# Kernel tuning notes

Hardware: AMD Instinct MI355X
Metric: run time of the kernel (lower is better)

The kernel has to match this reference:

```python
import jax, jax.numpy as jnp
import numpy as np

HID = 1024
HEADS = 16
HEAD_DIM = HID // HEADS
FF = 4096
CAP = 0.125
AUXW = 0.01
ROPE_THETA = 10000.0


def setup_inputs() -> dict:
    key = jax.random.key(0)
    ks = jax.random.split(key, 12)
    B, T, D = 4, 4096, HID
    s = 0.02  # weight init scale
    return {
        "hidden_states": jax.random.normal(ks[0], (B, T, D), jnp.float32),
        "w_router": jax.random.normal(ks[1], (D, 1), jnp.float32) * s,
        "wq": jax.random.normal(ks[2], (D, D), jnp.float32) * s,
        "wk": jax.random.normal(ks[3], (D, D), jnp.float32) * s,
        "wv": jax.random.normal(ks[4], (D, D), jnp.float32) * s,
        "wo": jax.random.normal(ks[5], (D, D), jnp.float32) * s,
        "ln1_w": jnp.ones((D,), jnp.float32),
        "ln2_w": jnp.ones((D,), jnp.float32),
        "w_gate": jax.random.normal(ks[6], (D, FF), jnp.float32) * s,
        "w_up": jax.random.normal(ks[7], (D, FF), jnp.float32) * s,
        "w_down": jax.random.normal(ks[8], (FF, D), jnp.float32) * s,
    }


def _rmsnorm(x, w, eps=1e-6):
    var = jnp.mean(jnp.square(x), axis=-1, keepdims=True)
    return x * jax.lax.rsqrt(var + eps) * w


def _rope(x, pos):
    # x: [B,S,H,Dh], pos: [B,S] float positions (original token indices)
    Dh = x.shape[-1]
    inv_freq = 1.0 / (ROPE_THETA ** (jnp.arange(0, Dh, 2, dtype=jnp.float32) / Dh))
    ang = pos[..., None] * inv_freq            # [B,S,Dh/2]
    cos = jnp.cos(ang)[:, :, None, :]
    sin = jnp.sin(ang)[:, :, None, :]
    x1, x2 = x[..., : Dh // 2], x[..., Dh // 2:]
    return jnp.concatenate([x1 * cos - x2 * sin, x2 * cos + x1 * sin], axis=-1)


def reference(hidden_states, w_router, wq, wk, wv, wo, ln1_w, ln2_w, w_gate, w_up, w_down):
    B, T, D = hidden_states.shape
    kk = max(1, int(T * CAP))  # tokens selected per row (static)

    # ---- router ----
    logits = (hidden_states @ w_router)[..., 0]          # [B,T]
    _, topi = jax.lax.top_k(logits, kk)                  # [B,kk]
    bidx = jnp.arange(B)[:, None]
    # aux loss: BCE-with-logits vs binary top-k targets, mean over all B*T
    targets = jnp.zeros_like(logits).at[bidx, topi].set(1.0)
    aux_loss = jnp.mean(
        jnp.maximum(logits, 0.0) - logits * targets + jnp.log1p(jnp.exp(-jnp.abs(logits)))
    ) * AUXW

    # ---- select tokens (sorted by position to preserve causality) ----
    idx = jnp.sort(topi, axis=-1)                        # [B,kk]
    x_sel = hidden_states[bidx, idx]                     # [B,kk,D]
    gates = jax.nn.sigmoid(logits[bidx, idx])[..., None] # [B,kk,1]
    pos = idx.astype(jnp.float32)

    # ---- decoder block on selected tokens ----
    h = _rmsnorm(x_sel, ln1_w)
    q = (h @ wq).reshape(B, kk, HEADS, HEAD_DIM)
    k = (h @ wk).reshape(B, kk, HEADS, HEAD_DIM)
    v = (h @ wv).reshape(B, kk, HEADS, HEAD_DIM)
    q = _rope(q, pos)
    k = _rope(k, pos)
    scores = jnp.einsum("bqhd,bkhd->bhqk", q, k) / np.sqrt(HEAD_DIM)
    causal = jnp.tril(jnp.ones((kk, kk), dtype=bool))
    scores = jnp.where(causal, scores, jnp.finfo(scores.dtype).min)
    attn = jax.nn.softmax(scores, axis=-1)
    o = jnp.einsum("bhqk,bkhd->bqhd", attn, v).reshape(B, kk, D) @ wo
    x1 = x_sel + o
    h2 = _rmsnorm(x1, ln2_w)
    mlp = (jax.nn.silu(h2 @ w_gate) * (h2 @ w_up)) @ w_down
    block_out = x1 + mlp

    # ---- soft-gated scatter back ----
    new_sel = x_sel + gates * (block_out - x_sel)
    new_states = hidden_states.at[bidx, idx].set(new_sel)
    return new_states, aux_loss
```

## Files before the change

kernel.cpp:

```cpp
#include <hip/hip_runtime.h>
#include <math.h>

#define NB 4
#define NT 4096
#define ND 1024
#define NH 16
#define NDH 64
#define NFF 4096
#define NKK 512
#define NTOK (NB*NKK)
#define OUT_MAIN ((size_t)NB*NT*ND)

typedef unsigned short u16;
typedef __bf16 bf16x8 __attribute__((ext_vector_type(8)));
typedef short  s16x8  __attribute__((ext_vector_type(8)));
typedef unsigned short u16x4 __attribute__((ext_vector_type(4)));
typedef float  f32x4  __attribute__((ext_vector_type(4)));

__device__ inline u16 f2b(float f) {
    unsigned u = __builtin_bit_cast(unsigned, f);
    unsigned r = u + 0x7FFFu + ((u >> 16) & 1u);
    return (u16)(r >> 16);
}
__device__ inline float b2f(u16 v) {
    unsigned u = ((unsigned)v) << 16;
    return __builtin_bit_cast(float, u);
}

__global__ __launch_bounds__(256)
void router_kernel(const float* __restrict__ hs, const float* __restrict__ wr,
                   float* __restrict__ logits, float* __restrict__ partials)
{
    int wave = threadIdx.x >> 6, lane = threadIdx.x & 63;
    int row = blockIdx.x * 4 + wave;
    const float4* x4 = (const float4*)(hs + (size_t)row * ND);
    const float4* w4 = (const float4*)wr;
    float acc = 0.f;
#pragma unroll
    for (int i = 0; i < 4; ++i) {
        float4 a = x4[lane + i * 64];
        float4 b = w4[lane + i * 64];
        acc += a.x * b.x + a.y * b.y + a.z * b.z + a.w * b.w;
    }
    for (int off = 32; off; off >>= 1) acc += __shfl_down(acc, off);
    __shared__ float sp4[4];
    if (lane == 0) {
        logits[row] = acc;
        sp4[wave] = fmaxf(acc, 0.f) + log1pf(expf(-fabsf(acc)));
    }
    __syncthreads();
    if (threadIdx.x == 0)
        partials[blockIdx.x] = sp4[0] + sp4[1] + sp4[2] + sp4[3];
}

__global__ __launch_bounds__(1024)
void topk_kernel(const float* __restrict__ logits, int* __restrict__ idxv,
                 float* __restrict__ gates, float* __restrict__ S2)
{
    __shared__ unsigned key[NT];
    __shared__ unsigned hist[256];
    __shared__ unsigned wsum[16];
    __shared__ float red[16];
    __shared__ unsigned sh_pref, sh_r;
    int b = blockIdx.x, tid = threadIdx.x;
    int lane = tid & 63, wv = tid >> 6;
    const float* lg = logits + (size_t)b * NT;
    for (int i = tid; i < NT; i += 1024) {
        unsigned u = __float_as_uint(lg[i]);
        u ^= (u >> 31) ? 0xFFFFFFFFu : 0x80000000u;
        key[i] = u;
    }
    if (tid == 0) { sh_pref = 0u; sh_r = NKK; }
    if (tid < 256) hist[tid] = 0u;
    __syncthreads();
    unsigned prefmask = 0u;
#pragma unroll
    for (int pass = 0; pass < 4; ++pass) {
        int shift = 24 - 8 * pass;
        unsigned pm = prefmask, pref = sh_pref;
        for (int i = tid; i < NT; i += 1024) {
            unsigned kk = key[i];
            if ((kk & pm) == pref) atomicAdd(&hist[(kk >> shift) & 255u], 1u);
        }
        __syncthreads();
        if (tid == 0) {
            unsigned r = sh_r, cum = 0;
            for (int bin = 255; bin >= 0; --bin) {
                unsigned c = hist[bin];
                if (cum + c >= r) {
                    sh_pref = pref | ((unsigned)bin << shift);
                    sh_r = r - cum;
                    break;
                }
                cum += c;
            }
        }
        __syncthreads();
        if (tid < 256) hist[tid] = 0u;
        prefmask |= (255u << shift);
        __syncthreads();
    }
    unsigned kstar = sh_pref;
    unsigned r2 = sh_r;
    int base = tid * 4;
    unsigned g_loc[4], t_loc[4];
    unsigned tsum = 0;
#pragma unroll
    for (int j = 0; j < 4; ++j) {
        unsigned kk = key[base + j];
        g_loc[j] = (kk > kstar) ? 1u : 0u;
        t_loc[j] = (kk == kstar) ? 1u : 0u;
        tsum += t_loc[j];
    }
    unsigned x = tsum;
#pragma unroll
    for (int off = 1; off < 64; off <<= 1) {
        unsigned v = __shfl_up(x, off);
        if (lane >= off) x += v;
    }
    if (lane == 63) wsum[wv] = x;
    __syncthreads();
    if (tid == 0) {
        unsigned run = 0;
        for (int i = 0; i < 16; ++i) { unsigned t = wsum[i]; wsum[i] = run; run += t; }
    }
    __syncthreads();
    unsigned tie_run = wsum[wv] + x - tsum;
    unsigned s_loc[4], ssum = 0;
#pragma unroll
    for (int j = 0; j < 4; ++j) {
        unsigned sel = g_loc[j] | (t_loc[j] & ((tie_run < r2) ? 1u : 0u));
        tie_run += t_loc[j];
        s_loc[j] = sel;
        ssum += sel;
    }
    __syncthreads();
    unsigned y = ssum;
#pragma unroll
    for (int off = 1; off < 64; off <<= 1) {
        unsigned v = __shfl_up(y, off);
        if (lane >= off) y += v;
    }
    if (lane == 63) wsum[wv] = y;
    __syncthreads();
    if (tid == 0) {
        unsigned run = 0;
        for (int i = 0; i < 16; ++i) { unsigned t = wsum[i]; wsum[i] = run; run += t; }
    }
    __syncthreads();
    unsigned pos = wsum[wv] + y - ssum;
    float lsum = 0.f;
#pragma unroll
    for (int j = 0; j < 4; ++j) {
        if (s_loc[j]) {
            int gi = base + j;
            float l = lg[gi];
            idxv[b * NKK + pos] = gi;
            gates[b * NKK + pos] = 1.f / (1.f + expf(-l));
            lsum += l;
            ++pos;
        }
    }
    for (int off = 32; off; off >>= 1) lsum += __shfl_down(lsum, off);
    if (lane == 0) red[wv] = lsum;
    __syncthreads();
    if (tid == 0) {
        float t = 0.f;
        for (int i = 0; i < 16; ++i) t += red[i];
        atomicAdd(S2, t);
    }
}

__global__ __launch_bounds__(1024)
void aux_kernel(const float* __restrict__ partials, const float* __restrict__ S2,
                float* __restrict__ outp)
{
    int tid = threadIdx.x, lane = tid & 63, wv = tid >> 6;
    float s = 0.f;
    for (int i = tid; i < 4096; i += 1024) s += partials[i];
    for (int off = 32; off; off >>= 1) s += __shfl_down(s, off);
    __shared__ float red[16];
    if (lane == 0) red[wv] = s;
    __syncthreads();
    if (tid == 0) {
        float t = 0.f;
        for (int i = 0; i < 16; ++i) t += red[i];
        outp[0] = (t - S2[0]) * (0.01f / (float)(NB * NT));
    }
}

__global__ __launch_bounds__(256)
void transpose_conv(const float* __restrict__ src, u16* __restrict__ dst,
                    int K, int N)
{
    __shared__ u16 T[64][68];
    int n0 = blockIdx.x * 64, k0 = blockIdx.y * 64;
    int tid = threadIdx.x;
#pragma unroll
    for (int it = 0; it < 4; ++it) {
        int slot = it * 256 + tid;
        int k = slot >> 4, n4 = (slot & 15) * 4;
        float4 v = *(const float4*)&src[(size_t)(k0 + k) * N + n0 + n4];
        u16x4 o = { f2b(v.x), f2b(v.y), f2b(v.z), f2b(v.w) };
        *(u16x4*)&T[k][n4] = o;
    }
    __syncthreads();
#pragma unroll
    for (int it = 0; it < 2; ++it) {
        int slot = it * 256 + tid;
        int n = slot >> 3, k8 = (slot & 7) * 8;
        s16x8 o;
#pragma unroll
        for (int i = 0; i < 8; ++i) o[i] = (short)T[k8 + i][n];
        *(s16x8*)&dst[(size_t)(n0 + n) * K + k0 + k8] = o;
    }
}

template<int GATHER>
__global__ __launch_bounds__(256)
void rms_kernel(const float* __restrict__ src, const int* __restrict__ idxv,
                const float* __restrict__ w, float* __restrict__ xsel,
                u16* __restrict__ outp)
{
    int blk = blockIdx.x, tid = threadIdx.x;
    const float* x;
    if (GATHER) {
        int b = blk >> 9;
        x = src + ((size_t)b * NT + idxv[blk]) * ND;
    } else {
        x = src + (size_t)blk * ND;
    }
    float4 v = *(const float4*)&x[tid * 4];
    float ss = v.x * v.x + v.y * v.y + v.z * v.z + v.w * v.w;
    for (int off = 32; off; off >>= 1) ss += __shfl_down(ss, off);
    __shared__ float wred[4];
    if ((tid & 63) == 0) wred[tid >> 6] = ss;
    __syncthreads();
    float tot = wred[0] + wred[1] + wred[2] + wred[3];
    float scale = rsqrtf(tot * (1.f / (float)ND) + 1e-6f);
    float4 wv = *(const float4*)&w[tid * 4];
    u16x4 o = { f2b(v.x * scale * wv.x), f2b(v.y * scale * wv.y),
                f2b(v.z * scale * wv.z), f2b(v.w * scale * wv.w) };
    *(u16x4*)&outp[(size_t)blk * ND + tid * 4] = o;
    if (GATHER) *(float4*)&xsel[(size_t)blk * ND + tid * 4] = v;
}

#define LPAD 40
template<int EPI>
__global__ __launch_bounds__(256)
void gemm_bt(const u16* __restrict__ A, const u16* __restrict__ B,
             void* __restrict__ Cv, int K, int lda, int ldb, int ldc,
             const float* __restrict__ P1, const float* __restrict__ P2,
             const float* __restrict__ gates, const int* __restrict__ idxv,
             float* __restrict__ outp)
{
    __shared__ u16 As[128 * LPAD];
    __shared__ u16 Bs[128 * LPAD];
    int tid = threadIdx.x, lane = tid & 63, w = tid >> 6;
    int wr = w >> 1, wc = w & 1;
    int bm = blockIdx.y * 128, bn = blockIdx.x * 128;
    int arow = tid >> 2, acol = (tid & 3) * 8;
    const u16* Ap = A + (size_t)(bm + arow) * lda + acol;
    const u16* Ap2 = Ap + (size_t)64 * lda;
    const u16* Bp = B + (size_t)(bn + arow) * ldb + acol;
    const u16* Bp2 = Bp + (size_t)64 * ldb;
    int c15 = lane & 15, ks8 = (lane >> 4) * 8;
    int aoff[4], boff[4];
#pragma unroll
    for (int m2 = 0; m2 < 4; ++m2) aoff[m2] = (wr * 64 + m2 * 16 + c15) * LPAD + ks8;
#pragma unroll
    for (int n2 = 0; n2 < 4; ++n2) boff[n2] = (wc * 64 + n2 * 16 + c15) * LPAD + ks8;
    f32x4 acc[4][4] = {};
    for (int k0 = 0; k0 < K; k0 += 32) {
        s16x8 a0 = *(const s16x8*)(Ap + k0);
        s16x8 a1 = *(const s16x8*)(Ap2 + k0);
        s16x8 b0 = *(const s16x8*)(Bp + k0);
        s16x8 b1 = *(const s16x8*)(Bp2 + k0);
        __syncthreads();
        *(s16x8*)&As[arow * LPAD + acol] = a0;
        *(s16x8*)&As[(arow + 64) * LPAD + acol] = a1;
        *(s16x8*)&Bs[arow * LPAD + acol] = b0;
        *(s16x8*)&Bs[(arow + 64) * LPAD + acol] = b1;
        __syncthreads();
        bf16x8 af[4], bfr[4];
#pragma unroll
        for (int m2 = 0; m2 < 4; ++m2) af[m2] = *(const bf16x8*)&As[aoff[m2]];
#pragma unroll
        for (int n2 = 0; n2 < 4; ++n2) bfr[n2] = *(const bf16x8*)&Bs[boff[n2]];
#pragma unroll
        for (int m2 = 0; m2 < 4; ++m2)
#pragma unroll
            for (int n2 = 0; n2 < 4; ++n2)
                acc[m2][n2] = __builtin_amdgcn_mfma_f32_16x16x32_bf16(
                    af[m2], bfr[n2], acc[m2][n2], 0, 0, 0);
    }
    int r4 = (lane >> 4) * 4;
#pragma unroll
    for (int m2 = 0; m2 < 4; ++m2) {
#pragma unroll
        for (int n2 = 0; n2 < 4; ++n2) {
            f32x4 v = acc[m2][n2];
            int c = bn + wc * 64 + n2 * 16 + c15;
            int r0 = bm + wr * 64 + m2 * 16 + r4;
#pragma unroll
            for (int j = 0; j < 4; ++j) {
                int r = r0 + j;
                float val = v[j];
                if (EPI == 1) {
                    ((u16*)Cv)[(size_t)r * ldc + c] = f2b(val);
                } else if (EPI == 2) {
                    ((float*)Cv)[(size_t)r * ldc + c] = val + P1[(size_t)r * ldc + c];
                } else {
                    float x1v = P1[(size_t)r * ND + c];
                    float xs  = P2[(size_t)r * ND + c];
                    float g = gates[r];
                    float ns = xs + g * (x1v + val - xs);
                    int bb = r >> 9;
                    int tok = idxv[r];
                    outp[((size_t)bb * NT + tok) * ND + c] = ns;
                }
            }
        }
    }
}

__global__ __launch_bounds__(256)
void rope_kernel(u16* __restrict__ qkv, const int* __restrict__ idxv)
{
    int row = blockIdx.x;
    float pos = (float)idxv[row];
    int tid = threadIdx.x;
    for (int p = tid; p < 1024; p += 256) {
        int sec = p >> 9, h = (p >> 5) & 15, j = p & 31;
        float inv = expf(-(float)j * 0.28782313662f);
        float ang = pos * inv;
        float s = sinf(ang), c = cosf(ang);
        size_t base = (size_t)row * 3072 + sec * 1024 + h * 64 + j;
        float x1 = b2f(qkv[base]), x2 = b2f(qkv[base + 32]);
        qkv[base] = f2b(x1 * c - x2 * s);
        qkv[base + 32] = f2b(x2 * c + x1 * s);
    }
}

__global__ __launch_bounds__(256)
void flash_attn(const u16* __restrict__ qkv, u16* __restrict__ ao)
{
    __shared__ u16 Qs[128 * 72];
    __shared__ u16 Ks[64 * 72];
    __shared__ u16 Vt[64 * 72];
    __shared__ u16 Ps[128 * 72];
    int qt = blockIdx.x, h = blockIdx.y, b = blockIdx.z;
    int tid = threadIdx.x, lane = tid & 63, w = tid >> 6;
    size_t rowbase = (size_t)b * NKK;
    int c15 = lane & 15, ks8 = (lane >> 4) * 8, r4 = (lane >> 4) * 4;
#pragma unroll
    for (int it = 0; it < 4; ++it) {
        int slot = it * 256 + tid;
        int r = slot >> 3, c8 = (slot & 7) * 8;
        s16x8 qv = *(const s16x8*)&qkv[(rowbase + qt * 128 + r) * 3072 + h * 64 + c8];
        *(s16x8*)&Qs[r * 72 + c8] = qv;
    }
    float m_run[2][4], l_run[2][4];
#pragma unroll
    for (int m2 = 0; m2 < 2; ++m2)
#pragma unroll
        for (int j = 0; j < 4; ++j) { m_run[m2][j] = -1e30f; l_run[m2][j] = 0.f; }
    f32x4 oacc[2][4] = {};
    int q0w = qt * 128 + w * 32;
    int nkt = (qt + 1) * 2;
    for (int kt = 0; kt < nkt; ++kt) {
        __syncthreads();
#pragma unroll
        for (int it = 0; it < 2; ++it) {
            int slot = it * 256 + tid;
            int r = slot >> 3, c8 = (slot & 7) * 8;
            s16x8 kv_ = *(const s16x8*)&qkv[(rowbase + kt * 64 + r) * 3072 + 1024 + h * 64 + c8];
            *(s16x8*)&Ks[r * 72 + c8] = kv_;
        }
#pragma unroll
        for (int it = 0; it < 2; ++it) {
            int slot = it * 256 + tid;
            int r = slot >> 3, c8 = (slot & 7) * 8;
            s16x8 vv = *(const s16x8*)&qkv[(rowbase + kt * 64 + r) * 3072 + 2048 + h * 64 + c8];
#pragma unroll
            for (int i = 0; i < 8; ++i) Vt[(c8 + i) * 72 + r] = (u16)vv[i];
        }
        __syncthreads();
        if (kt * 64 <= q0w + 31) {
            f32x4 sacc[2][4] = {};
#pragma unroll
            for (int ks = 0; ks < 2; ++ks) {
                bf16x8 af[2], bfr[4];
#pragma unroll
                for (int m2 = 0; m2 < 2; ++m2)
                    af[m2] = *(const bf16x8*)&Qs[(w * 32 + m2 * 16 + c15) * 72 + ks * 32 + ks8];
#pragma unroll
                for (int n2 = 0; n2 < 4; ++n2)
                    bfr[n2] = *(const bf16x8*)&Ks[(n2 * 16 + c15) * 72 + ks * 32 + ks8];
#pragma unroll
                for (int m2 = 0; m2 < 2; ++m2)
#pragma unroll
                    for (int n2 = 0; n2 < 4; ++n2)
                        sacc[m2][n2] = __builtin_amdgcn_mfma_f32_16x16x32_bf16(
                            af[m2], bfr[n2], sacc[m2][n2], 0, 0, 0);
            }
#pragma unroll
            for (int m2 = 0; m2 < 2; ++m2) {
#pragma unroll
                for (int j = 0; j < 4; ++j) {
                    int rowv = q0w + m2 * 16 + r4 + j;
                    float sv[4];
#pragma unroll
                    for (int n2 = 0; n2 < 4; ++n2) {
                        int colv = kt * 64 + n2 * 16 + c15;
                        float s = sacc[m2][n2][j] * 0.125f;
                        sv[n2] = (colv > rowv) ? -1e30f : s;
                    }
                    float mx = fmaxf(fmaxf(sv[0], sv[1]), fmaxf(sv[2], sv[3]));
                    mx = fmaxf(mx, __shfl_xor(mx, 1));
                    mx = fmaxf(mx, __shfl_xor(mx, 2));
                    mx = fmaxf(mx, __shfl_xor(mx, 4));
                    mx = fmaxf(mx, __shfl_xor(mx, 8));
                    float newm = fmaxf(m_run[m2][j], mx);
                    float alpha = __expf(m_run[m2][j] - newm);
                    m_run[m2][j] = newm;
                    float ls = 0.f;
                    int prow = w * 32 + m2 * 16 + r4 + j;
#pragma unroll
                    for (int n2 = 0; n2 < 4; ++n2) {
                        float pexp = __expf(sv[n2] - newm);
                        ls += pexp;
                        Ps[prow * 72 + n2 * 16 + c15] = f2b(pexp);
                    }
                    ls += __shfl_xor(ls, 1);
                    ls += __shfl_xor(ls, 2);
                    ls += __shfl_xor(ls, 4);
                    ls += __shfl_xor(ls, 8);
                    l_run[m2][j] = l_run[m2][j] * alpha + ls;
#pragma unroll
                    for (int n2 = 0; n2 < 4; ++n2) oacc[m2][n2][j] *= alpha;
                }
            }
#pragma unroll
            for (int ks = 0; ks < 2; ++ks) {
                bf16x8 pa[2], vb[4];
#pragma unroll
                for (int m2 = 0; m2 < 2; ++m2)
                    pa[m2] = *(const bf16x8*)&Ps[(w * 32 + m2 * 16 + c15) * 72 + ks * 32 + ks8];
#pragma unroll
                for (int n2 = 0; n2 < 4; ++n2)
                    vb[n2] = *(const bf16x8*)&Vt[(n2 * 16 + c15) * 72 + ks * 32 + ks8];
#pragma unroll
                for (int m2 = 0; m2 < 2; ++m2)
#pragma unroll
                    for (int n2 = 0; n2 < 4; ++n2)
                        oacc[m2][n2] = __builtin_amdgcn_mfma_f32_16x16x32_bf16(
                            pa[m2], vb[n2], oacc[m2][n2], 0, 0, 0);
            }
        }
    }
#pragma unroll
    for (int m2 = 0; m2 < 2; ++m2) {
#pragma unroll
        for (int j = 0; j < 4; ++j) {
            float invl = 1.f / l_run[m2][j];
            size_t r = rowbase + q0w + m2 * 16 + r4 + j;
#pragma unroll
            for (int n2 = 0; n2 < 4; ++n2)
                ao[r * ND + h * 64 + n2 * 16 + c15] = f2b(oacc[m2][n2][j] * invl);
        }
    }
}

__global__ __launch_bounds__(256)
void dual_gemm_silu(const u16* __restrict__ A, const u16* __restrict__ Bw,
                    u16* __restrict__ act)
{
    __shared__ u16 As[128 * LPAD];
    __shared__ u16 Bg[64 * LPAD];
    __shared__ u16 Bu[64 * LPAD];
    int tid = threadIdx.x, lane = tid & 63, w = tid >> 6;
    int bm = blockIdx.y * 128, bn = blockIdx.x * 64;
    int arow = tid >> 2, acol = (tid & 3) * 8;
    const u16* Ap = A + (size_t)(bm + arow) * ND + acol;
    const u16* Ap2 = Ap + (size_t)64 * ND;
    const u16* Gp = Bw + (size_t)(bn + arow) * ND + acol;
    const u16* Up = Bw + (size_t)(NFF + bn + arow) * ND + acol;
    int c15 = lane & 15, ks8 = (lane >> 4) * 8;
    int aoff[2], boff[4];
#pragma unroll
    for (int m2 = 0; m2 < 2; ++m2) aoff[m2] = (w * 32 + m2 * 16 + c15) * LPAD + ks8;
#pragma unroll
    for (int n2 = 0; n2 < 4; ++n2) boff[n2] = (n2 * 16 + c15) * LPAD + ks8;
    f32x4 accg[2][4] = {}, accu[2][4] = {};
    for (int k0 = 0; k0 < ND; k0 += 32) {
        s16x8 a0 = *(const s16x8*)(Ap + k0);
        s16x8 a1 = *(const s16x8*)(Ap2 + k0);
        s16x8 g0 = *(const s16x8*)(Gp + k0);
        s16x8 u0 = *(const s16x8*)(Up + k0);
        __syncthreads();
        *(s16x8*)&As[arow * LPAD + acol] = a0;
        *(s16x8*)&As[(arow + 64) * LPAD + acol] = a1;
        *(s16x8*)&Bg[arow * LPAD + acol] = g0;
        *(s16x8*)&Bu[arow * LPAD + acol] = u0;
        __syncthreads();
        bf16x8 af[2], gf[4], uf[4];
#pragma unroll
        for (int m2 = 0; m2 < 2; ++m2) af[m2] = *(const bf16x8*)&As[aoff[m2]];
#pragma unroll
        for (int n2 = 0; n2 < 4; ++n2) { gf[n2] = *(const bf16x8*)&Bg[boff[n2]];
                                         uf[n2] = *(const bf16x8*)&Bu[boff[n2]]; }
#pragma unroll
        for (int m2 = 0; m2 < 2; ++m2)
#pragma unroll
            for (int n2 = 0; n2 < 4; ++n2) {
                accg[m2][n2] = __builtin_amdgcn_mfma_f32_16x16x32_bf16(
                    af[m2], gf[n2], accg[m2][n2], 0, 0, 0);
                accu[m2][n2] = __builtin_amdgcn_mfma_f32_16x16x32_bf16(
                    af[m2], uf[n2], accu[m2][n2], 0, 0, 0);
            }
    }
    int r4 = (lane >> 4) * 4;
#pragma unroll
    for (int m2 = 0; m2 < 2; ++m2)
#pragma unroll
        for (int n2 = 0; n2 < 4; ++n2)
#pragma unroll
            for (int j = 0; j < 4; ++j) {
                float g = accg[m2][n2][j], uu = accu[m2][n2][j];
                float a = g / (1.f + __expf(-g)) * uu;
                int r = bm + w * 32 + m2 * 16 + r4 + j;
                int c = bn + n2 * 16 + c15;
                act[(size_t)r * NFF + c] = f2b(a);
            }
}

extern "C" void kernel_launch(void* const* d_in, const int* in_sizes, int n_in,
                              void* d_out, int out_size, void* d_ws, size_t ws_size,
                              hipStream_t stream)
{
    const float* hs  = (const float*)d_in[0];
    const float* wr  = (const float*)d_in[1];
    const float* wq  = (const float*)d_in[2];
    const float* wk  = (const float*)d_in[3];
    const float* wv  = (const float*)d_in[4];
    const float* wo  = (const float*)d_in[5];
    const float* ln1 = (const float*)d_in[6];
    const float* ln2 = (const float*)d_in[7];
    const float* wg  = (const float*)d_in[8];
    const float* wu  = (const float*)d_in[9];
    const float* wd  = (const float*)d_in[10];
    float* out = (float*)d_out;
    char* w8 = (char*)d_ws;

    float* logits   = (float*)w8;
    float* partials = logits + 16384;
    float* S2       = partials + 4096;
    int*   idxv  = (int*)(w8 + 0x20000);
    float* gates = (float*)(w8 + 0x22000);
    float* xsel  = (float*)(w8 + 0x30000);
    float* x1b   = xsel + (size_t)NTOK * ND;
    u16*   hbuf  = (u16*)(x1b + (size_t)NTOK * ND);
    u16*   wqkvT = hbuf + (size_t)NTOK * ND;
    u16*   woT   = wqkvT + (size_t)3072 * 1024;
    u16*   wguT  = woT + (size_t)1024 * 1024;
    u16*   wdT   = wguT + (size_t)8192 * 1024;
    u16*   act   = wdT + (size_t)1024 * 4096;
    u16*   qkv   = act + (size_t)NTOK * NFF;
    u16*   ao    = qkv + (size_t)NTOK * 3072;

    hipMemcpyAsync(out, hs, OUT_MAIN * sizeof(float), hipMemcpyDeviceToDevice, stream);
    hipMemsetAsync(S2, 0, sizeof(float), stream);

    transpose_conv<<<dim3(16, 16), 256, 0, stream>>>(wq, wqkvT, 1024, 1024);
    transpose_conv<<<dim3(16, 16), 256, 0, stream>>>(wk, wqkvT + (size_t)1024 * 1024, 1024, 1024);
    transpose_conv<<<dim3(16, 16), 256, 0, stream>>>(wv, wqkvT + (size_t)2048 * 1024, 1024, 1024);
    transpose_conv<<<dim3(16, 16), 256, 0, stream>>>(wo, woT, 1024, 1024);
    transpose_conv<<<dim3(64, 16), 256, 0, stream>>>(wg, wguT, 1024, 4096);
    transpose_conv<<<dim3(64, 16), 256, 0, stream>>>(wu, wguT + (size_t)4096 * 1024, 1024, 4096);
    transpose_conv<<<dim3(16, 64), 256, 0, stream>>>(wd, wdT, 4096, 1024);

    router_kernel<<<NB * NT / 4, 256, 0, stream>>>(hs, wr, logits, partials);
    topk_kernel<<<NB, 1024, 0, stream>>>(logits, idxv, gates, S2);
    aux_kernel<<<1, 1024, 0, stream>>>(partials, S2, out + OUT_MAIN);

    rms_kernel<1><<<NTOK, 256, 0, stream>>>(hs, idxv, ln1, xsel, hbuf);

    gemm_bt<1><<<dim3(24, 16), 256, 0, stream>>>(
        hbuf, wqkvT, qkv, 1024, 1024, 1024, 3072,
        nullptr, nullptr, nullptr, nullptr, nullptr);

    rope_kernel<<<NTOK, 256, 0, stream>>>(qkv, idxv);

    flash_attn<<<dim3(4, NH, NB), 256, 0, stream>>>(qkv, ao);

    gemm_bt<2><<<dim3(8, 16), 256, 0, stream>>>(
        ao, woT, x1b, 1024, 1024, 1024, 1024,
        xsel, nullptr, nullptr, nullptr, nullptr);

    rms_kernel<0><<<NTOK, 256, 0, stream>>>(x1b, idxv, ln2, nullptr, hbuf);

    dual_gemm_silu<<<dim3(64, 16), 256, 0, stream>>>(hbuf, wguT, act);

    gemm_bt<3><<<dim3(8, 16), 256, 0, stream>>>(
        act, wdT, nullptr, 4096, 4096, 4096, 1024,
        x1b, xsel, gates, idxv, out);
}
```

Baseline: 513.4 us.

## Swizzle LDS layouts in GEMMs and attention, narrow N tile for small GEMMs

Replaces padded shared-memory rows with XOR-swizzled unpadded layouts in the GEMM, dual SiLU GEMM and flash attention kernels, aiming to avoid LDS bank conflicts while using less shared memory. Also templates the GEMM on the N tile width and uses 64-wide tiles for the output-projection and down-projection GEMMs, doubling their grid from 128 to 256 blocks to fill more CUs. The swizzle index arithmetic adds some integer work, and the narrower tiles reduce data reuse per block.

```diff
diff --git a/kernel.cpp b/kernel.cpp
--- a/kernel.cpp
+++ b/kernel.cpp
@@ -26,6 +26,9 @@
     unsigned u = ((unsigned)v) << 16;
     return __builtin_bit_cast(float, u);
 }
+
+__device__ inline int swzA(int r, int s) { return r * 32 + (((s ^ (r >> 1)) & 3) << 3); }
+__device__ inline int swz64(int r, int s) { return r * 64 + (((s ^ r) & 7) << 3); }
 
 __global__ __launch_bounds__(256)
 void router_kernel(const float* __restrict__ hs, const float* __restrict__ wr,
@@ -245,8 +248,7 @@
     if (GATHER) *(float4*)&xsel[(size_t)blk * ND + tid * 4] = v;
 }
 
-#define LPAD 40
-template<int EPI>
+template<int EPI, int BN>
 __global__ __launch_bounds__(256)
 void gemm_bt(const u16* __restrict__ A, const u16* __restrict__ B,
              void* __restrict__ Cv, int K, int lda, int ldb, int ldc,
@@ -254,43 +256,46 @@
              const float* __restrict__ gates, const int* __restrict__ idxv,
              float* __restrict__ outp)
 {
-    __shared__ u16 As[128 * LPAD];
-    __shared__ u16 Bs[128 * LPAD];
+    constexpr int NF = BN / 32;
+    __shared__ u16 As[128 * 32];
+    __shared__ u16 Bs[BN * 32];
     int tid = threadIdx.x, lane = tid & 63, w = tid >> 6;
     int wr = w >> 1, wc = w & 1;
-    int bm = blockIdx.y * 128, bn = blockIdx.x * 128;
-    int arow = tid >> 2, acol = (tid & 3) * 8;
-    const u16* Ap = A + (size_t)(bm + arow) * lda + acol;
+    int bm = blockIdx.y * 128, bn = blockIdx.x * BN;
+    int arow = tid >> 2, g = tid & 3;
+    const u16* Ap  = A + (size_t)(bm + arow) * lda + g * 8;
     const u16* Ap2 = Ap + (size_t)64 * lda;
-    const u16* Bp = B + (size_t)(bn + arow) * ldb + acol;
+    const u16* Bp  = B + (size_t)(bn + arow) * ldb + g * 8;
     const u16* Bp2 = Bp + (size_t)64 * ldb;
-    int c15 = lane & 15, ks8 = (lane >> 4) * 8;
-    int aoff[4], boff[4];
-#pragma unroll
-    for (int m2 = 0; m2 < 4; ++m2) aoff[m2] = (wr * 64 + m2 * 16 + c15) * LPAD + ks8;
-#pragma unroll
-    for (int n2 = 0; n2 < 4; ++n2) boff[n2] = (wc * 64 + n2 * 16 + c15) * LPAD + ks8;
-    f32x4 acc[4][4] = {};
+    int c15 = lane & 15, ksl = lane >> 4;
+    int aoff[4], boff[NF];
+#pragma unroll
+    for (int m2 = 0; m2 < 4; ++m2) aoff[m2] = swzA(wr * 64 + m2 * 16 + c15, ksl);
+#pragma unroll
+    for (int n2 = 0; n2 < NF; ++n2) boff[n2] = swzA(wc * 16 * NF + n2 * 16 + c15, ksl);
+    int wa0 = swzA(arow, g), wa1 = swzA(arow + 64, g);
+    f32x4 acc[4][NF] = {};
     for (int k0 = 0; k0 < K; k0 += 32) {
         s16x8 a0 = *(const s16x8*)(Ap + k0);
         s16x8 a1 = *(const s16x8*)(Ap2 + k0);
         s16x8 b0 = *(const s16x8*)(Bp + k0);
-        s16x8 b1 = *(const s16x8*)(Bp2 + k0);
-        __syncthreads();
-        *(s16x8*)&As[arow * LPAD + acol] = a0;
-        *(s16x8*)&As[(arow + 64) * LPAD + acol] = a1;
-        *(s16x8*)&Bs[arow * LPAD + acol] = b0;
-        *(s16x8*)&Bs[(arow + 64) * LPAD + acol] = b1;
-        __syncthreads();
-        bf16x8 af[4], bfr[4];
+        s16x8 b1;
+        if (BN == 128) b1 = *(const s16x8*)(Bp2 + k0);
+        __syncthreads();
+        *(s16x8*)&As[wa0] = a0;
+        *(s16x8*)&As[wa1] = a1;
+        *(s16x8*)&Bs[wa0] = b0;
+        if (BN == 128) *(s16x8*)&Bs[wa1] = b1;
+        __syncthreads();
+        bf16x8 af[4], bfr[NF];
 #pragma unroll
         for (int m2 = 0; m2 < 4; ++m2) af[m2] = *(const bf16x8*)&As[aoff[m2]];
 #pragma unroll
-        for (int n2 = 0; n2 < 4; ++n2) bfr[n2] = *(const bf16x8*)&Bs[boff[n2]];
+        for (int n2 = 0; n2 < NF; ++n2) bfr[n2] = *(const bf16x8*)&Bs[boff[n2]];
 #pragma unroll
         for (int m2 = 0; m2 < 4; ++m2)
 #pragma unroll
-            for (int n2 = 0; n2 < 4; ++n2)
+            for (int n2 = 0; n2 < NF; ++n2)
                 acc[m2][n2] = __builtin_amdgcn_mfma_f32_16x16x32_bf16(
                     af[m2], bfr[n2], acc[m2][n2], 0, 0, 0);
     }
@@ -298,9 +303,9 @@
 #pragma unroll
     for (int m2 = 0; m2 < 4; ++m2) {
 #pragma unroll
-        for (int n2 = 0; n2 < 4; ++n2) {
+        for (int n2 = 0; n2 < NF; ++n2) {
             f32x4 v = acc[m2][n2];
-            int c = bn + wc * 64 + n2 * 16 + c15;
+            int c = bn + wc * 16 * NF + n2 * 16 + c15;
             int r0 = bm + wr * 64 + m2 * 16 + r4;
 #pragma unroll
             for (int j = 0; j < 4; ++j) {
@@ -313,8 +318,8 @@
                 } else {
                     float x1v = P1[(size_t)r * ND + c];
                     float xs  = P2[(size_t)r * ND + c];
-                    float g = gates[r];
-                    float ns = xs + g * (x1v + val - xs);
+                    float gt = gates[r];
+                    float ns = xs + gt * (x1v + val - xs);
                     int bb = r >> 9;
                     int tok = idxv[r];
                     outp[((size_t)bb * NT + tok) * ND + c] = ns;
@@ -345,20 +350,20 @@
 __global__ __launch_bounds__(256)
 void flash_attn(const u16* __restrict__ qkv, u16* __restrict__ ao)
 {
-    __shared__ u16 Qs[128 * 72];
-    __shared__ u16 Ks[64 * 72];
-    __shared__ u16 Vt[64 * 72];
-    __shared__ u16 Ps[128 * 72];
+    __shared__ u16 Qs[128 * 64];
+    __shared__ u16 Ks[64 * 64];
+    __shared__ u16 Vt[64 * 64];
+    __shared__ u16 Ps[128 * 64];
     int qt = blockIdx.x, h = blockIdx.y, b = blockIdx.z;
     int tid = threadIdx.x, lane = tid & 63, w = tid >> 6;
     size_t rowbase = (size_t)b * NKK;
-    int c15 = lane & 15, ks8 = (lane >> 4) * 8, r4 = (lane >> 4) * 4;
+    int c15 = lane & 15, ksl = lane >> 4, r4 = (lane >> 4) * 4;
 #pragma unroll
     for (int it = 0; it < 4; ++it) {
         int slot = it * 256 + tid;
-        int r = slot >> 3, c8 = (slot & 7) * 8;
-        s16x8 qv = *(const s16x8*)&qkv[(rowbase + qt * 128 + r) * 3072 + h * 64 + c8];
-        *(s16x8*)&Qs[r * 72 + c8] = qv;
+        int r = slot >> 3, s = slot & 7;
+        s16x8 qv = *(const s16x8*)&qkv[(rowbase + qt * 128 + r) * 3072 + h * 64 + s * 8];
+        *(s16x8*)&Qs[swz64(r, s)] = qv;
     }
     float m_run[2][4], l_run[2][4];
 #pragma unroll
@@ -373,17 +378,20 @@
 #pragma unroll
         for (int it = 0; it < 2; ++it) {
             int slot = it * 256 + tid;
-            int r = slot >> 3, c8 = (slot & 7) * 8;
-            s16x8 kv_ = *(const s16x8*)&qkv[(rowbase + kt * 64 + r) * 3072 + 1024 + h * 64 + c8];
-            *(s16x8*)&Ks[r * 72 + c8] = kv_;
+            int r = slot >> 3, s = slot & 7;
+            s16x8 kv_ = *(const s16x8*)&qkv[(rowbase + kt * 64 + r) * 3072 + 1024 + h * 64 + s * 8];
+            *(s16x8*)&Ks[swz64(r, s)] = kv_;
         }
 #pragma unroll
         for (int it = 0; it < 2; ++it) {
             int slot = it * 256 + tid;
-            int r = slot >> 3, c8 = (slot & 7) * 8;
-            s16x8 vv = *(const s16x8*)&qkv[(rowbase + kt * 64 + r) * 3072 + 2048 + h * 64 + c8];
-#pragma unroll
-            for (int i = 0; i < 8; ++i) Vt[(c8 + i) * 72 + r] = (u16)vv[i];
+            int r = slot >> 3, s = slot & 7;
+            s16x8 vv = *(const s16x8*)&qkv[(rowbase + kt * 64 + r) * 3072 + 2048 + h * 64 + s * 8];
+#pragma unroll
+            for (int i = 0; i < 8; ++i) {
+                int vr = s * 8 + i;
+                Vt[vr * 64 + ((((r >> 3) ^ vr) & 7) << 3) + (r & 7)] = (u16)vv[i];
+            }
         }
         __syncthreads();
         if (kt * 64 <= q0w + 31) {
@@ -393,10 +401,10 @@
                 bf16x8 af[2], bfr[4];
 #pragma unroll
                 for (int m2 = 0; m2 < 2; ++m2)
-                    af[m2] = *(const bf16x8*)&Qs[(w * 32 + m2 * 16 + c15) * 72 + ks * 32 + ks8];
+                    af[m2] = *(const bf16x8*)&Qs[swz64(w * 32 + m2 * 16 + c15, ks * 4 + ksl)];
 #pragma unroll
                 for (int n2 = 0; n2 < 4; ++n2)
-                    bfr[n2] = *(const bf16x8*)&Ks[(n2 * 16 + c15) * 72 + ks * 32 + ks8];
+                    bfr[n2] = *(const bf16x8*)&Ks[swz64(n2 * 16 + c15, ks * 4 + ksl)];
 #pragma unroll
                 for (int m2 = 0; m2 < 2; ++m2)
 #pragma unroll
@@ -430,7 +438,8 @@
                     for (int n2 = 0; n2 < 4; ++n2) {
                         float pexp = __expf(sv[n2] - newm);
                         ls += pexp;
-                        Ps[prow * 72 + n2 * 16 + c15] = f2b(pexp);
+                        int c = n2 * 16 + c15;
+                        Ps[prow * 64 + ((((c >> 3) ^ prow) & 7) << 3) + (c & 7)] = f2b(pexp);
                     }
                     ls += __shfl_xor(ls, 1);
                     ls += __shfl_xor(ls, 2);
@@ -446,10 +455,10 @@
                 bf16x8 pa[2], vb[4];
 #pragma unroll
                 for (int m2 = 0; m2 < 2; ++m2)
-                    pa[m2] = *(const bf16x8*)&Ps[(w * 32 + m2 * 16 + c15) * 72 + ks * 32 + ks8];
+                    pa[m2] = *(const bf16x8*)&Ps[swz64(w * 32 + m2 * 16 + c15, ks * 4 + ksl)];
 #pragma unroll
                 for (int n2 = 0; n2 < 4; ++n2)
-                    vb[n2] = *(const bf16x8*)&Vt[(n2 * 16 + c15) * 72 + ks * 32 + ks8];
+                    vb[n2] = *(const bf16x8*)&Vt[swz64(n2 * 16 + c15, ks * 4 + ksl)];
 #pragma unroll
                 for (int m2 = 0; m2 < 2; ++m2)
 #pragma unroll
@@ -476,22 +485,23 @@
 void dual_gemm_silu(const u16* __restrict__ A, const u16* __restrict__ Bw,
                     u16* __restrict__ act)
 {
-    __shared__ u16 As[128 * LPAD];
-    __shared__ u16 Bg[64 * LPAD];
-    __shared__ u16 Bu[64 * LPAD];
+    __shared__ u16 As[128 * 32];
+    __shared__ u16 Bg[64 * 32];
+    __shared__ u16 Bu[64 * 32];
     int tid = threadIdx.x, lane = tid & 63, w = tid >> 6;
     int bm = blockIdx.y * 128, bn = blockIdx.x * 64;
-    int arow = tid >> 2, acol = (tid & 3) * 8;
-    const u16* Ap = A + (size_t)(bm + arow) * ND + acol;
+    int arow = tid >> 2, g = tid & 3;
+    const u16* Ap  = A + (size_t)(bm + arow) * ND + g * 8;
     const u16* Ap2 = Ap + (size_t)64 * ND;
-    const u16* Gp = Bw + (size_t)(bn + arow) * ND + acol;
-    const u16* Up = Bw + (size_t)(NFF + bn + arow) * ND + acol;
-    int c15 = lane & 15, ks8 = (lane >> 4) * 8;
+    const u16* Gp  = Bw + (size_t)(bn + arow) * ND + g * 8;
+    const u16* Up  = Bw + (size_t)(NFF + bn + arow) * ND + g * 8;
+    int c15 = lane & 15, ksl = lane >> 4;
     int aoff[2], boff[4];
 #pragma unroll
-    for (int m2 = 0; m2 < 2; ++m2) aoff[m2] = (w * 32 + m2 * 16 + c15) * LPAD + ks8;
-#pragma unroll
-    for (int n2 = 0; n2 < 4; ++n2) boff[n2] = (n2 * 16 + c15) * LPAD + ks8;
+    for (int m2 = 0; m2 < 2; ++m2) aoff[m2] = swzA(w * 32 + m2 * 16 + c15, ksl);
+#pragma unroll
+    for (int n2 = 0; n2 < 4; ++n2) boff[n2] = swzA(n2 * 16 + c15, ksl);
+    int wa0 = swzA(arow, g), wa1 = swzA(arow + 64, g);
     f32x4 accg[2][4] = {}, accu[2][4] = {};
     for (int k0 = 0; k0 < ND; k0 += 32) {
         s16x8 a0 = *(const s16x8*)(Ap + k0);
@@ -499,10 +509,10 @@
         s16x8 g0 = *(const s16x8*)(Gp + k0);
         s16x8 u0 = *(const s16x8*)(Up + k0);
         __syncthreads();
-        *(s16x8*)&As[arow * LPAD + acol] = a0;
-        *(s16x8*)&As[(arow + 64) * LPAD + acol] = a1;
-        *(s16x8*)&Bg[arow * LPAD + acol] = g0;
-        *(s16x8*)&Bu[arow * LPAD + acol] = u0;
+        *(s16x8*)&As[wa0] = a0;
+        *(s16x8*)&As[wa1] = a1;
+        *(s16x8*)&Bg[wa0] = g0;
+        *(s16x8*)&Bu[wa0] = u0;
         __syncthreads();
         bf16x8 af[2], gf[4], uf[4];
 #pragma unroll
@@ -527,8 +537,8 @@
         for (int n2 = 0; n2 < 4; ++n2)
 #pragma unroll
             for (int j = 0; j < 4; ++j) {
-                float g = accg[m2][n2][j], uu = accu[m2][n2][j];
-                float a = g / (1.f + __expf(-g)) * uu;
+                float gg = accg[m2][n2][j], uu = accu[m2][n2][j];
+                float a = gg / (1.f + __expf(-gg)) * uu;
                 int r = bm + w * 32 + m2 * 16 + r4 + j;
                 int c = bn + n2 * 16 + c15;
                 act[(size_t)r * NFF + c] = f2b(a);
@@ -586,7 +596,7 @@
 
     rms_kernel<1><<<NTOK, 256, 0, stream>>>(hs, idxv, ln1, xsel, hbuf);
 
-    gemm_bt<1><<<dim3(24, 16), 256, 0, stream>>>(
+    gemm_bt<1, 128><<<dim3(24, 16), 256, 0, stream>>>(
         hbuf, wqkvT, qkv, 1024, 1024, 1024, 3072,
         nullptr, nullptr, nullptr, nullptr, nullptr);
 
@@ -594,7 +604,7 @@
 
     flash_attn<<<dim3(4, NH, NB), 256, 0, stream>>>(qkv, ao);
 
-    gemm_bt<2><<<dim3(8, 16), 256, 0, stream>>>(
+    gemm_bt<2, 64><<<dim3(16, 16), 256, 0, stream>>>(
         ao, woT, x1b, 1024, 1024, 1024, 1024,
         xsel, nullptr, nullptr, nullptr, nullptr);
 
@@ -602,7 +612,7 @@
 
     dual_gemm_silu<<<dim3(64, 16), 256, 0, stream>>>(hbuf, wguT, act);
 
-    gemm_bt<3><<<dim3(8, 16), 256, 0, stream>>>(
+    gemm_bt<3, 64><<<dim3(16, 16), 256, 0, stream>>>(
         act, wdT, nullptr, 4096, 4096, 4096, 1024,
         x1b, xsel, gates, idxv, out);
 }
```

New measurement: 486.2 us. 5.3% less time.
